# Performance work log

Hardware: AMD Instinct MI355X
Metric: run time of the kernel (lower is better)

Reference implementation:

```python
import jax, jax.numpy as jnp
import numpy as np

L, H, D, E, V, MAXS = 12, 12, 64, 768, 50257, 1024

def _ln(x, g, b, eps=1e-5):
    m = jnp.mean(x, axis=-1, keepdims=True)
    v = jnp.mean(jnp.square(x - m), axis=-1, keepdims=True)
    return (x - m) * jax.lax.rsqrt(v + eps) * g + b

def setup_inputs() -> dict:
    key = jax.random.key(0)
    ks = jax.random.split(key, 16)
    s = 0.02
    inp = {
        "input_ids": jax.random.randint(ks[0], (1, 1), 0, V),
        "past_key": jax.random.normal(ks[1], (L, 1, H, MAXS, D), jnp.float32),
        "past_value": jax.random.normal(ks[2], (L, 1, H, MAXS, D), jnp.float32),
        "past_seq_len": 1023,
        "attention_mask": jnp.ones((1, MAXS), jnp.float32),
        "wte": jax.random.normal(ks[3], (V, E), jnp.float32) * s,
        "wpe": jax.random.normal(ks[4], (MAXS, E), jnp.float32) * s,
        "ln1_g": jnp.ones((L, E), jnp.float32),
        "ln1_b": jnp.zeros((L, E), jnp.float32),
        "attn_w": jax.random.normal(ks[5], (L, E, 3 * E), jnp.float32) * s,
        "attn_b": jnp.zeros((L, 3 * E), jnp.float32),
        "proj_w": jax.random.normal(ks[6], (L, E, E), jnp.float32) * s,
        "proj_b": jnp.zeros((L, E), jnp.float32),
        "ln2_g": jnp.ones((L, E), jnp.float32),
        "ln2_b": jnp.zeros((L, E), jnp.float32),
        "fc_w": jax.random.normal(ks[7], (L, E, 4 * E), jnp.float32) * s,
        "fc_b": jnp.zeros((L, 4 * E), jnp.float32),
        "mlp_w": jax.random.normal(ks[8], (L, 4 * E, E), jnp.float32) * s,
        "mlp_b": jnp.zeros((L, E), jnp.float32),
        "lnf_g": jnp.ones((E,), jnp.float32),
        "lnf_b": jnp.zeros((E,), jnp.float32),
    }
    return inp

def reference(input_ids, past_key, past_value, past_seq_len, attention_mask,
              wte, wpe, ln1_g, ln1_b, attn_w, attn_b, proj_w, proj_b,
              ln2_g, ln2_b, fc_w, fc_b, mlp_w, mlp_b, lnf_g, lnf_b):
    S = int(past_seq_len)  # static cache length
    h = wte[input_ids] + wpe[S]                      # [1,1,E]
    bias = (1.0 - attention_mask[:, :S + 1]) * -1e9  # [1,S+1]
    scale = 1.0 / jnp.sqrt(jnp.float32(D))
    pk, pv = past_key, past_value
    for l in range(L):
        x = _ln(h, ln1_g[l], ln1_b[l])
        qkv = x @ attn_w[l] + attn_b[l]              # [1,1,3E]
        q, k, v = jnp.split(qkv, 3, axis=-1)
        q = q.reshape(1, 1, H, D).transpose(0, 2, 1, 3)  # [1,H,1,D]
        k = k.reshape(1, 1, H, D).transpose(0, 2, 1, 3)
        v = v.reshape(1, 1, H, D).transpose(0, 2, 1, 3)
        k_full = jnp.concatenate([pk[l, :, :, :S, :], k], axis=2)  # [1,H,S+1,D]
        v_full = jnp.concatenate([pv[l, :, :, :S, :], v], axis=2)
        scores = jnp.einsum('bhqd,bhkd->bhqk', q, k_full) * scale
        scores = scores + bias[:, None, None, :]
        attn = jax.nn.softmax(scores, axis=-1)
        o = jnp.einsum('bhqk,bhkd->bhqd', attn, v_full)
        o = o.transpose(0, 2, 1, 3).reshape(1, 1, H * D)
        h = h + o @ proj_w[l] + proj_b[l]
        x2 = _ln(h, ln2_g[l], ln2_b[l])
        h = h + jax.nn.gelu(x2 @ fc_w[l] + fc_b[l], approximate=True) @ mlp_w[l] + mlp_b[l]
        pk = pk.at[l, :, :, S, :].set(k[:, :, 0, :])
        pv = pv.at[l, :, :, S, :].set(v[:, :, 0, :])
    h = _ln(h, lnf_g, lnf_b)
    logits = h @ wte.T                               # [1,1,V] (tied lm_head)
    return (logits, pk, pv)
```

## Files before the change

### kernel.cpp

```cpp
#include <hip/hip_runtime.h>
#include <math.h>

#define EMB 768
#define NH 12
#define HD 64
#define NL 12
#define NV 50257
#define MAXS 1024
#define S_PAST 1023
#define E3 2304
#define E4 3072

#define WS_H    0
#define WS_QKV  768
#define WS_FC   3072
#define WS_PART 6144

__device__ __forceinline__ void blockReduce2(float& a, float& b, volatile float* ra, volatile float* rb) {
  int lane = threadIdx.x & 63, wid = threadIdx.x >> 6;
#pragma unroll
  for (int o = 32; o > 0; o >>= 1) { a += __shfl_down(a, o); b += __shfl_down(b, o); }
  if (lane == 0) { ra[wid] = a; rb[wid] = b; }
  __syncthreads();
  if (threadIdx.x == 0) {
    ra[0] = ra[0] + ra[1] + ra[2] + ra[3];
    rb[0] = rb[0] + rb[1] + rb[2] + rb[3];
  }
  __syncthreads();
  a = ra[0]; b = rb[0];
}

__global__ void embed_kernel(const int* __restrict__ ids, const float* __restrict__ wte,
                             const float* __restrict__ wpe, const float* __restrict__ attn_b,
                             float* __restrict__ hvec, float* __restrict__ qkv) {
  int idx = blockIdx.x * 256 + threadIdx.x;
  if (idx < E3) qkv[idx] = attn_b[idx];
  if (idx < EMB) {
    int id = ids[0];
    hvec[idx] = wte[(size_t)id * EMB + idx] + wpe[(size_t)S_PAST * EMB + idx];
  }
}

__global__ void ln_gemv4(const float* __restrict__ hvec, const float* __restrict__ g,
                         const float* __restrict__ bb, const float* __restrict__ W,
                         float* __restrict__ out, int N, int l) {
  __shared__ float lh[EMB];
  __shared__ float xs[64];
  __shared__ float ra[4], rb[4];
  __shared__ float4 red[4][64];
  int tid = threadIdx.x, lane = tid & 63, wid = tid >> 6;
  float s1 = 0.f, s2 = 0.f;
  for (int e = tid; e < EMB; e += 256) { float v = hvec[e]; lh[e] = v; s1 += v; s2 += v * v; }
  blockReduce2(s1, s2, ra, rb);
  float mean = s1 * (1.f / EMB);
  float var = s2 * (1.f / EMB) - mean * mean;
  float rstd = rsqrtf(var + 1e-5f);
  int e0 = blockIdx.y * 64;
  if (tid < 64) {
    int e = e0 + tid;
    xs[tid] = (lh[e] - mean) * rstd * g[l * EMB + e] + bb[l * EMB + e];
  }
  __syncthreads();
  int j4 = blockIdx.x * 64 + lane;
  int N4 = N >> 2;
  const float4* W4 = (const float4*)(W + (size_t)l * EMB * N) + (size_t)e0 * N4 + j4;
  const float4* p = W4 + (size_t)wid * N4;
  float4 w[16];
#pragma unroll
  for (int i = 0; i < 16; i++) w[i] = p[(size_t)(i * 4) * N4];
  float4 acc = {0.f, 0.f, 0.f, 0.f};
#pragma unroll
  for (int i = 0; i < 16; i++) {
    float x = xs[wid + i * 4];
    acc.x += x * w[i].x; acc.y += x * w[i].y; acc.z += x * w[i].z; acc.w += x * w[i].w;
  }
  red[wid][lane] = acc;
  __syncthreads();
  if (wid == 0) {
    float4 a0 = red[0][lane], a1 = red[1][lane], a2 = red[2][lane], a3 = red[3][lane];
    float rx = a0.x + a1.x + a2.x + a3.x;
    float ry = a0.y + a1.y + a2.y + a3.y;
    float rz = a0.z + a1.z + a2.z + a3.z;
    float rw = a0.w + a1.w + a2.w + a3.w;
    float* op = out + (size_t)j4 * 4;
    atomicAdd(op + 0, rx); atomicAdd(op + 1, ry);
    atomicAdd(op + 2, rz); atomicAdd(op + 3, rw);
  }
}

__global__ void attn_kv(const float* __restrict__ qkv, const float* __restrict__ pk,
                        const float* __restrict__ pv, const float* __restrict__ mask,
                        float* __restrict__ opk, float* __restrict__ opv,
                        float* __restrict__ part, int l) {
  int h = blockIdx.x >> 3, c = blockIdx.x & 7;
  int tid = threadIdx.x, lane = tid & 63, wid = tid >> 6;
  int sub = tid & 15, grp = tid >> 4;
  __shared__ float4 qs4[16];
  __shared__ float sc[128];
  __shared__ float4 redo[4][16];
  if (tid < 16) qs4[tid] = ((const float4*)(qkv + h * 64))[tid];
  __syncthreads();
  size_t base = ((size_t)(l * NH + h) * MAXS) * HD;
  const float4* K4 = (const float4*)(pk + base);
  const float4* V4 = (const float4*)(pv + base);
  float4* oK4 = (float4*)(opk + base);
  float4* oV4 = (float4*)(opv + base);
  int t0 = c * 128;
  float4 kreg[8];
#pragma unroll
  for (int i = 0; i < 8; i++) {
    int t = t0 + grp + i * 16;
    kreg[i] = (t == S_PAST) ? ((const float4*)(qkv + EMB + h * 64))[sub] : K4[(size_t)t * 16 + sub];
  }
#pragma unroll
  for (int i = 0; i < 8; i++) {
    int t = t0 + grp + i * 16;
    oK4[(size_t)t * 16 + sub] = kreg[i];
  }
  float4 q4 = qs4[sub];
#pragma unroll
  for (int i = 0; i < 8; i++) {
    int key = grp + i * 16;
    float p = q4.x * kreg[i].x + q4.y * kreg[i].y + q4.z * kreg[i].z + q4.w * kreg[i].w;
    p += __shfl_xor(p, 1); p += __shfl_xor(p, 2);
    p += __shfl_xor(p, 4); p += __shfl_xor(p, 8);
    if (sub == 0) sc[key] = p * 0.125f + (1.f - mask[t0 + key]) * (-1e9f);
  }
  __syncthreads();
  if (wid == 0) {
    float a = sc[lane], b2 = sc[lane + 64];
    float m = fmaxf(a, b2);
#pragma unroll
    for (int o = 32; o > 0; o >>= 1) m = fmaxf(m, __shfl_down(m, o));
    m = __shfl(m, 0);
    float ea = expf(a - m), eb = expf(b2 - m);
    sc[lane] = ea; sc[lane + 64] = eb;
    float s = ea + eb;
#pragma unroll
    for (int o = 32; o > 0; o >>= 1) s += __shfl_down(s, o);
    if (lane == 0) { part[(h * 8 + c) * 68 + 0] = m; part[(h * 8 + c) * 68 + 1] = s; }
  }
  __syncthreads();
  float4 vreg[8];
#pragma unroll
  for (int i = 0; i < 8; i++) {
    int t = t0 + grp + i * 16;
    vreg[i] = (t == S_PAST) ? ((const float4*)(qkv + 2 * EMB + h * 64))[sub] : V4[(size_t)t * 16 + sub];
  }
#pragma unroll
  for (int i = 0; i < 8; i++) {
    int t = t0 + grp + i * 16;
    oV4[(size_t)t * 16 + sub] = vreg[i];
  }
  float4 acc = {0.f, 0.f, 0.f, 0.f};
#pragma unroll
  for (int i = 0; i < 8; i++) {
    float w = sc[grp + i * 16];
    acc.x += w * vreg[i].x; acc.y += w * vreg[i].y; acc.z += w * vreg[i].z; acc.w += w * vreg[i].w;
  }
  acc.x += __shfl_xor(acc.x, 16); acc.y += __shfl_xor(acc.y, 16);
  acc.z += __shfl_xor(acc.z, 16); acc.w += __shfl_xor(acc.w, 16);
  acc.x += __shfl_xor(acc.x, 32); acc.y += __shfl_xor(acc.y, 32);
  acc.z += __shfl_xor(acc.z, 32); acc.w += __shfl_xor(acc.w, 32);
  if (lane < 16) redo[wid][lane] = acc;
  __syncthreads();
  if (tid < 16) {
    float4 a0 = redo[0][tid], a1 = redo[1][tid], a2 = redo[2][tid], a3 = redo[3][tid];
    float4 r;
    r.x = a0.x + a1.x + a2.x + a3.x;
    r.y = a0.y + a1.y + a2.y + a3.y;
    r.z = a0.z + a1.z + a2.z + a3.z;
    r.w = a0.w + a1.w + a2.w + a3.w;
    ((float4*)(part + (h * 8 + c) * 68 + 4))[tid] = r;
  }
}

__global__ void proj_attn(const float* __restrict__ part, const float* __restrict__ W,
                          const float* __restrict__ bias, const float* __restrict__ fc_b,
                          float* __restrict__ hout, float* __restrict__ wfc, int l) {
  int jb = blockIdx.x;
  int h = blockIdx.y;
  int tid = threadIdx.x, lane = tid & 63, wid = tid >> 6;
  __shared__ float xs[64];
  __shared__ float4 red[4][64];
  if (tid < 64) {
    float M = -1e30f;
    for (int cc = 0; cc < 8; cc++) M = fmaxf(M, part[(h * 8 + cc) * 68]);
    float T = 0.f, o = 0.f;
    for (int cc = 0; cc < 8; cc++) {
      float w = expf(part[(h * 8 + cc) * 68] - M);
      T += part[(h * 8 + cc) * 68 + 1] * w;
      o += part[(h * 8 + cc) * 68 + 4 + tid] * w;
    }
    xs[tid] = o / T;
  }
  int bid = h * 3 + jb;
  if (bid < 12) wfc[bid * 256 + tid] = fc_b[l * E4 + bid * 256 + tid];
  __syncthreads();
  int j4 = jb * 64 + lane;
  const int N4 = EMB >> 2;
  const float4* W4 = (const float4*)(W + (size_t)l * EMB * EMB) + (size_t)(h * 64) * N4 + j4;
  const float4* p = W4 + (size_t)wid * N4;
  float4 w[16];
#pragma unroll
  for (int i = 0; i < 16; i++) w[i] = p[(size_t)(i * 4) * N4];
  float4 acc = {0.f, 0.f, 0.f, 0.f};
#pragma unroll
  for (int i = 0; i < 16; i++) {
    float x = xs[wid + i * 4];
    acc.x += x * w[i].x; acc.y += x * w[i].y; acc.z += x * w[i].z; acc.w += x * w[i].w;
  }
  red[wid][lane] = acc;
  __syncthreads();
  if (wid == 0) {
    float4 a0 = red[0][lane], a1 = red[1][lane], a2 = red[2][lane], a3 = red[3][lane];
    float rx = a0.x + a1.x + a2.x + a3.x;
    float ry = a0.y + a1.y + a2.y + a3.y;
    float rz = a0.z + a1.z + a2.z + a3.z;
    float rw = a0.w + a1.w + a2.w + a3.w;
    if (h == 0) {
      const float* bp = bias + l * EMB + j4 * 4;
      rx += bp[0]; ry += bp[1]; rz += bp[2]; rw += bp[3];
    }
    float* op = hout + (size_t)j4 * 4;
    atomicAdd(op + 0, rx); atomicAdd(op + 1, ry);
    atomicAdd(op + 2, rz); atomicAdd(op + 3, rw);
  }
}

__global__ void mlp_gemv4(const float* __restrict__ fcv, const float* __restrict__ W,
                          const float* __restrict__ bias, const float* __restrict__ attn_b,
                          float* __restrict__ hout, float* __restrict__ qkv, int l) {
  __shared__ float xs[128];
  __shared__ float4 red[4][64];
  int tid = threadIdx.x, lane = tid & 63, wid = tid >> 6;
  int e0 = blockIdx.y * 128;
  if (tid < 128) {
    float x = fcv[e0 + tid];
    xs[tid] = 0.5f * x * (1.f + tanhf(0.7978845608028654f * (x + 0.044715f * x * x * x)));
  }
  int bid = blockIdx.y * 3 + blockIdx.x;
  if (l + 1 < NL && bid < 9) qkv[bid * 256 + tid] = attn_b[(l + 1) * E3 + bid * 256 + tid];
  __syncthreads();
  int j4 = blockIdx.x * 64 + lane;
  const int N4 = EMB >> 2;
  const float4* W4 = (const float4*)(W + (size_t)l * E4 * EMB) + (size_t)e0 * N4 + j4;
  float4 acc = {0.f, 0.f, 0.f, 0.f};
#pragma unroll
  for (int b = 0; b < 2; b++) {
    const float4* p = W4 + (size_t)(b * 64 + wid) * N4;
    float4 w[16];
#pragma unroll
    for (int i = 0; i < 16; i++) w[i] = p[(size_t)(i * 4) * N4];
#pragma unroll
    for (int i = 0; i < 16; i++) {
      float x = xs[b * 64 + wid + i * 4];
      acc.x += x * w[i].x; acc.y += x * w[i].y; acc.z += x * w[i].z; acc.w += x * w[i].w;
    }
  }
  red[wid][lane] = acc;
  __syncthreads();
  if (wid == 0) {
    float4 a0 = red[0][lane], a1 = red[1][lane], a2 = red[2][lane], a3 = red[3][lane];
    float rx = a0.x + a1.x + a2.x + a3.x;
    float ry = a0.y + a1.y + a2.y + a3.y;
    float rz = a0.z + a1.z + a2.z + a3.z;
    float rw = a0.w + a1.w + a2.w + a3.w;
    if (blockIdx.y == 0) {
      const float* bp = bias + l * EMB + j4 * 4;
      rx += bp[0]; ry += bp[1]; rz += bp[2]; rw += bp[3];
    }
    float* op = hout + (size_t)j4 * 4;
    atomicAdd(op + 0, rx); atomicAdd(op + 1, ry);
    atomicAdd(op + 2, rz); atomicAdd(op + 3, rw);
  }
}

__global__ void logits_lnf(const float* __restrict__ hvec, const float* __restrict__ g,
                           const float* __restrict__ b, const float* __restrict__ wte,
                           float* __restrict__ out) {
  __shared__ float4 xs4[192];
  __shared__ float ra[4], rb[4];
  int tid = threadIdx.x, lane = tid & 63, wid = tid >> 6;
  float s1 = 0.f, s2 = 0.f;
  float v0[3];
  int k = 0;
  for (int e = tid; e < EMB; e += 256, k++) { float v = hvec[e]; v0[k] = v; s1 += v; s2 += v * v; }
  blockReduce2(s1, s2, ra, rb);
  float mean = s1 * (1.f / EMB);
  float var = s2 * (1.f / EMB) - mean * mean;
  float rstd = rsqrtf(var + 1e-5f);
  k = 0;
  for (int e = tid; e < EMB; e += 256, k++)
    ((float*)xs4)[e] = (v0[k] - mean) * rstd * g[e] + b[e];
  __syncthreads();
  int v = blockIdx.x * 4 + wid;
  if (v >= NV) return;
  const float4* row = (const float4*)(wte + (size_t)v * EMB);
  float4 a0 = row[lane], a1 = row[lane + 64], a2 = row[lane + 128];
  float4 x0 = xs4[lane], x1 = xs4[lane + 64], x2 = xs4[lane + 128];
  float acc = a0.x * x0.x + a0.y * x0.y + a0.z * x0.z + a0.w * x0.w
            + a1.x * x1.x + a1.y * x1.y + a1.z * x1.z + a1.w * x1.w
            + a2.x * x2.x + a2.y * x2.y + a2.z * x2.z + a2.w * x2.w;
#pragma unroll
  for (int o = 32; o > 0; o >>= 1) acc += __shfl_down(acc, o);
  if (lane == 0) out[v] = acc;
}

extern "C" void kernel_launch(void* const* d_in, const int* in_sizes, int n_in,
                              void* d_out, int out_size, void* d_ws, size_t ws_size,
                              hipStream_t stream) {
  const int* input_ids = (const int*)d_in[0];
  const float* past_key = (const float*)d_in[1];
  const float* past_value = (const float*)d_in[2];
  const float* mask = (const float*)d_in[4];
  const float* wte = (const float*)d_in[5];
  const float* wpe = (const float*)d_in[6];
  const float* ln1_g = (const float*)d_in[7];
  const float* ln1_b = (const float*)d_in[8];
  const float* attn_w = (const float*)d_in[9];
  const float* attn_b = (const float*)d_in[10];
  const float* proj_w = (const float*)d_in[11];
  const float* proj_b = (const float*)d_in[12];
  const float* ln2_g = (const float*)d_in[13];
  const float* ln2_b = (const float*)d_in[14];
  const float* fc_w = (const float*)d_in[15];
  const float* fc_b = (const float*)d_in[16];
  const float* mlp_w = (const float*)d_in[17];
  const float* mlp_b = (const float*)d_in[18];
  const float* lnf_g = (const float*)d_in[19];
  const float* lnf_b = (const float*)d_in[20];

  float* out = (float*)d_out;
  float* out_logits = out;
  float* out_pk = out + NV;
  float* out_pv = out_pk + (size_t)NL * NH * MAXS * HD;

  float* ws = (float*)d_ws;
  float* wh = ws + WS_H;
  float* wqkv = ws + WS_QKV;
  float* wfc = ws + WS_FC;
  float* wpart = ws + WS_PART;

  embed_kernel<<<9, 256, 0, stream>>>(input_ids, wte, wpe, attn_b, wh, wqkv);

  for (int l = 0; l < NL; l++) {
    ln_gemv4<<<dim3(9, 12), 256, 0, stream>>>(wh, ln1_g, ln1_b, attn_w, wqkv, E3, l);
    attn_kv<<<96, 256, 0, stream>>>(wqkv, past_key, past_value, mask, out_pk, out_pv, wpart, l);
    proj_attn<<<dim3(3, 12), 256, 0, stream>>>(wpart, proj_w, proj_b, fc_b, wh, wfc, l);
    ln_gemv4<<<dim3(12, 12), 256, 0, stream>>>(wh, ln2_g, ln2_b, fc_w, wfc, E4, l);
    mlp_gemv4<<<dim3(3, 24), 256, 0, stream>>>(wfc, mlp_w, mlp_b, attn_b, wh, wqkv, l);
  }
  logits_lnf<<<12565, 256, 0, stream>>>(wh, lnf_g, lnf_b, wte, out_logits);
}
```

Before: 444.6 us.

## Bulk-copy KV cache upfront and split GEMV/attention across more blocks

Moves the full past KV cache copy into one bandwidth-bound kernel at the start, merged with the embedding setup. The per-layer attention kernel then only writes the new token's K/V row. All per-layer kernels (QKV, attention, projection, FC, MLP) now use smaller row chunks per block and roughly double or quadruple their grid sizes. This is meant to raise parallelism on the many CUs in the serial decode chain, at the cost of more atomic adds and partial results.

```diff
diff --git a/kernel.cpp b/kernel.cpp
--- a/kernel.cpp
+++ b/kernel.cpp
@@ -30,22 +30,39 @@
   a = ra[0]; b = rb[0];
 }
 
-__global__ void embed_kernel(const int* __restrict__ ids, const float* __restrict__ wte,
-                             const float* __restrict__ wpe, const float* __restrict__ attn_b,
-                             float* __restrict__ hvec, float* __restrict__ qkv) {
-  int idx = blockIdx.x * 256 + threadIdx.x;
-  if (idx < E3) qkv[idx] = attn_b[idx];
-  if (idx < EMB) {
-    int id = ids[0];
-    hvec[idx] = wte[(size_t)id * EMB + idx] + wpe[(size_t)S_PAST * EMB + idx];
-  }
-}
-
+__global__ void copy_embed(const float* __restrict__ pk, const float* __restrict__ pv,
+                           float* __restrict__ opk, float* __restrict__ opv,
+                           const int* __restrict__ ids, const float* __restrict__ wte,
+                           const float* __restrict__ wpe, const float* __restrict__ attn_b,
+                           float* __restrict__ hvec, float* __restrict__ qkv) {
+  int tid = threadIdx.x;
+  if (blockIdx.x >= 2048) {
+    int bi = blockIdx.x - 2048;
+    qkv[bi * 256 + tid] = attn_b[bi * 256 + tid];
+    if (bi < 3) {
+      int id = ids[0];
+      int e = bi * 256 + tid;
+      hvec[e] = wte[(size_t)id * EMB + e] + wpe[(size_t)S_PAST * EMB + e];
+    }
+    return;
+  }
+  const size_t n4 = (size_t)NL * NH * MAXS * HD / 4;
+  const float4* pk4 = (const float4*)pk;
+  const float4* pv4 = (const float4*)pv;
+  float4* opk4 = (float4*)opk;
+  float4* opv4 = (float4*)opv;
+  for (size_t i = (size_t)blockIdx.x * 256 + tid; i < n4; i += (size_t)2048 * 256) {
+    opk4[i] = pk4[i];
+    opv4[i] = pv4[i];
+  }
+}
+
+template<int R>
 __global__ void ln_gemv4(const float* __restrict__ hvec, const float* __restrict__ g,
                          const float* __restrict__ bb, const float* __restrict__ W,
                          float* __restrict__ out, int N, int l) {
   __shared__ float lh[EMB];
-  __shared__ float xs[64];
+  __shared__ float xs[R];
   __shared__ float ra[4], rb[4];
   __shared__ float4 red[4][64];
   int tid = threadIdx.x, lane = tid & 63, wid = tid >> 6;
@@ -55,22 +72,21 @@
   float mean = s1 * (1.f / EMB);
   float var = s2 * (1.f / EMB) - mean * mean;
   float rstd = rsqrtf(var + 1e-5f);
-  int e0 = blockIdx.y * 64;
-  if (tid < 64) {
+  int e0 = blockIdx.y * R;
+  if (tid < R) {
     int e = e0 + tid;
     xs[tid] = (lh[e] - mean) * rstd * g[l * EMB + e] + bb[l * EMB + e];
   }
   __syncthreads();
   int j4 = blockIdx.x * 64 + lane;
   int N4 = N >> 2;
-  const float4* W4 = (const float4*)(W + (size_t)l * EMB * N) + (size_t)e0 * N4 + j4;
-  const float4* p = W4 + (size_t)wid * N4;
-  float4 w[16];
-#pragma unroll
-  for (int i = 0; i < 16; i++) w[i] = p[(size_t)(i * 4) * N4];
+  const float4* p = (const float4*)(W + (size_t)l * EMB * N) + (size_t)e0 * N4 + j4 + (size_t)wid * N4;
+  float4 w[R / 4];
+#pragma unroll
+  for (int i = 0; i < R / 4; i++) w[i] = p[(size_t)(i * 4) * N4];
   float4 acc = {0.f, 0.f, 0.f, 0.f};
 #pragma unroll
-  for (int i = 0; i < 16; i++) {
+  for (int i = 0; i < R / 4; i++) {
     float x = xs[wid + i * 4];
     acc.x += x * w[i].x; acc.y += x * w[i].y; acc.z += x * w[i].z; acc.w += x * w[i].w;
   }
@@ -92,34 +108,29 @@
                         const float* __restrict__ pv, const float* __restrict__ mask,
                         float* __restrict__ opk, float* __restrict__ opv,
                         float* __restrict__ part, int l) {
-  int h = blockIdx.x >> 3, c = blockIdx.x & 7;
+  int h = blockIdx.x >> 4, c = blockIdx.x & 15;
   int tid = threadIdx.x, lane = tid & 63, wid = tid >> 6;
   int sub = tid & 15, grp = tid >> 4;
   __shared__ float4 qs4[16];
-  __shared__ float sc[128];
+  __shared__ float sc[64];
   __shared__ float4 redo[4][16];
   if (tid < 16) qs4[tid] = ((const float4*)(qkv + h * 64))[tid];
   __syncthreads();
   size_t base = ((size_t)(l * NH + h) * MAXS) * HD;
   const float4* K4 = (const float4*)(pk + base);
   const float4* V4 = (const float4*)(pv + base);
-  float4* oK4 = (float4*)(opk + base);
-  float4* oV4 = (float4*)(opv + base);
-  int t0 = c * 128;
-  float4 kreg[8];
-#pragma unroll
-  for (int i = 0; i < 8; i++) {
+  int t0 = c * 64;
+  float4 kreg[4];
+#pragma unroll
+  for (int i = 0; i < 4; i++) {
     int t = t0 + grp + i * 16;
     kreg[i] = (t == S_PAST) ? ((const float4*)(qkv + EMB + h * 64))[sub] : K4[(size_t)t * 16 + sub];
   }
-#pragma unroll
-  for (int i = 0; i < 8; i++) {
-    int t = t0 + grp + i * 16;
-    oK4[(size_t)t * 16 + sub] = kreg[i];
-  }
+  if (c == 15 && grp == 15)
+    ((float4*)(opk + base))[(size_t)S_PAST * 16 + sub] = kreg[3];
   float4 q4 = qs4[sub];
 #pragma unroll
-  for (int i = 0; i < 8; i++) {
+  for (int i = 0; i < 4; i++) {
     int key = grp + i * 16;
     float p = q4.x * kreg[i].x + q4.y * kreg[i].y + q4.z * kreg[i].z + q4.w * kreg[i].w;
     p += __shfl_xor(p, 1); p += __shfl_xor(p, 2);
@@ -128,33 +139,30 @@
   }
   __syncthreads();
   if (wid == 0) {
-    float a = sc[lane], b2 = sc[lane + 64];
-    float m = fmaxf(a, b2);
+    float a = sc[lane];
+    float m = a;
 #pragma unroll
     for (int o = 32; o > 0; o >>= 1) m = fmaxf(m, __shfl_down(m, o));
     m = __shfl(m, 0);
-    float ea = expf(a - m), eb = expf(b2 - m);
-    sc[lane] = ea; sc[lane + 64] = eb;
-    float s = ea + eb;
+    float ea = expf(a - m);
+    sc[lane] = ea;
+    float s = ea;
 #pragma unroll
     for (int o = 32; o > 0; o >>= 1) s += __shfl_down(s, o);
-    if (lane == 0) { part[(h * 8 + c) * 68 + 0] = m; part[(h * 8 + c) * 68 + 1] = s; }
-  }
-  __syncthreads();
-  float4 vreg[8];
-#pragma unroll
-  for (int i = 0; i < 8; i++) {
+    if (lane == 0) { part[(h * 16 + c) * 68 + 0] = m; part[(h * 16 + c) * 68 + 1] = s; }
+  }
+  __syncthreads();
+  float4 vreg[4];
+#pragma unroll
+  for (int i = 0; i < 4; i++) {
     int t = t0 + grp + i * 16;
     vreg[i] = (t == S_PAST) ? ((const float4*)(qkv + 2 * EMB + h * 64))[sub] : V4[(size_t)t * 16 + sub];
   }
-#pragma unroll
-  for (int i = 0; i < 8; i++) {
-    int t = t0 + grp + i * 16;
-    oV4[(size_t)t * 16 + sub] = vreg[i];
-  }
+  if (c == 15 && grp == 15)
+    ((float4*)(opv + base))[(size_t)S_PAST * 16 + sub] = vreg[3];
   float4 acc = {0.f, 0.f, 0.f, 0.f};
 #pragma unroll
-  for (int i = 0; i < 8; i++) {
+  for (int i = 0; i < 4; i++) {
     float w = sc[grp + i * 16];
     acc.x += w * vreg[i].x; acc.y += w * vreg[i].y; acc.z += w * vreg[i].z; acc.w += w * vreg[i].w;
   }
@@ -171,7 +179,7 @@
     r.y = a0.y + a1.y + a2.y + a3.y;
     r.z = a0.z + a1.z + a2.z + a3.z;
     r.w = a0.w + a1.w + a2.w + a3.w;
-    ((float4*)(part + (h * 8 + c) * 68 + 4))[tid] = r;
+    ((float4*)(part + (h * 16 + c) * 68 + 4))[tid] = r;
   }
 }
 
@@ -179,34 +187,38 @@
                           const float* __restrict__ bias, const float* __restrict__ fc_b,
                           float* __restrict__ hout, float* __restrict__ wfc, int l) {
   int jb = blockIdx.x;
-  int h = blockIdx.y;
-  int tid = threadIdx.x, lane = tid & 63, wid = tid >> 6;
-  __shared__ float xs[64];
+  int rt = blockIdx.y;
+  int h = rt >> 2, esub = rt & 3;
+  int tid = threadIdx.x, lane = tid & 63, wid = tid >> 6;
+  __shared__ float xs[16];
   __shared__ float4 red[4][64];
-  if (tid < 64) {
+  if (tid < 16) {
     float M = -1e30f;
-    for (int cc = 0; cc < 8; cc++) M = fmaxf(M, part[(h * 8 + cc) * 68]);
+#pragma unroll
+    for (int cc = 0; cc < 16; cc++) M = fmaxf(M, part[(h * 16 + cc) * 68]);
     float T = 0.f, o = 0.f;
-    for (int cc = 0; cc < 8; cc++) {
-      float w = expf(part[(h * 8 + cc) * 68] - M);
-      T += part[(h * 8 + cc) * 68 + 1] * w;
-      o += part[(h * 8 + cc) * 68 + 4 + tid] * w;
+    int d = esub * 16 + tid;
+#pragma unroll
+    for (int cc = 0; cc < 16; cc++) {
+      float w = expf(part[(h * 16 + cc) * 68] - M);
+      T += part[(h * 16 + cc) * 68 + 1] * w;
+      o += part[(h * 16 + cc) * 68 + 4 + d] * w;
     }
     xs[tid] = o / T;
   }
-  int bid = h * 3 + jb;
+  int bid = rt * 3 + jb;
   if (bid < 12) wfc[bid * 256 + tid] = fc_b[l * E4 + bid * 256 + tid];
   __syncthreads();
   int j4 = jb * 64 + lane;
   const int N4 = EMB >> 2;
-  const float4* W4 = (const float4*)(W + (size_t)l * EMB * EMB) + (size_t)(h * 64) * N4 + j4;
-  const float4* p = W4 + (size_t)wid * N4;
-  float4 w[16];
-#pragma unroll
-  for (int i = 0; i < 16; i++) w[i] = p[(size_t)(i * 4) * N4];
+  int r0 = h * 64 + esub * 16;
+  const float4* p = (const float4*)(W + (size_t)l * EMB * EMB) + (size_t)(r0 + wid) * N4 + j4;
+  float4 w[4];
+#pragma unroll
+  for (int i = 0; i < 4; i++) w[i] = p[(size_t)(i * 4) * N4];
   float4 acc = {0.f, 0.f, 0.f, 0.f};
 #pragma unroll
-  for (int i = 0; i < 16; i++) {
+  for (int i = 0; i < 4; i++) {
     float x = xs[wid + i * 4];
     acc.x += x * w[i].x; acc.y += x * w[i].y; acc.z += x * w[i].z; acc.w += x * w[i].w;
   }
@@ -218,11 +230,11 @@
     float ry = a0.y + a1.y + a2.y + a3.y;
     float rz = a0.z + a1.z + a2.z + a3.z;
     float rw = a0.w + a1.w + a2.w + a3.w;
-    if (h == 0) {
-      const float* bp = bias + l * EMB + j4 * 4;
+    if (rt == 0) {
+      const float* bp = bias + l * EMB + jb * 256 + lane * 4;
       rx += bp[0]; ry += bp[1]; rz += bp[2]; rw += bp[3];
     }
-    float* op = hout + (size_t)j4 * 4;
+    float* op = hout + (size_t)jb * 256 + (size_t)lane * 4;
     atomicAdd(op + 0, rx); atomicAdd(op + 1, ry);
     atomicAdd(op + 2, rz); atomicAdd(op + 3, rw);
   }
@@ -231,11 +243,11 @@
 __global__ void mlp_gemv4(const float* __restrict__ fcv, const float* __restrict__ W,
                           const float* __restrict__ bias, const float* __restrict__ attn_b,
                           float* __restrict__ hout, float* __restrict__ qkv, int l) {
-  __shared__ float xs[128];
+  __shared__ float xs[64];
   __shared__ float4 red[4][64];
   int tid = threadIdx.x, lane = tid & 63, wid = tid >> 6;
-  int e0 = blockIdx.y * 128;
-  if (tid < 128) {
+  int e0 = blockIdx.y * 64;
+  if (tid < 64) {
     float x = fcv[e0 + tid];
     xs[tid] = 0.5f * x * (1.f + tanhf(0.7978845608028654f * (x + 0.044715f * x * x * x)));
   }
@@ -244,19 +256,15 @@
   __syncthreads();
   int j4 = blockIdx.x * 64 + lane;
   const int N4 = EMB >> 2;
-  const float4* W4 = (const float4*)(W + (size_t)l * E4 * EMB) + (size_t)e0 * N4 + j4;
+  const float4* p = (const float4*)(W + (size_t)l * E4 * EMB) + (size_t)(e0 + wid) * N4 + j4;
+  float4 w[16];
+#pragma unroll
+  for (int i = 0; i < 16; i++) w[i] = p[(size_t)(i * 4) * N4];
   float4 acc = {0.f, 0.f, 0.f, 0.f};
 #pragma unroll
-  for (int b = 0; b < 2; b++) {
-    const float4* p = W4 + (size_t)(b * 64 + wid) * N4;
-    float4 w[16];
-#pragma unroll
-    for (int i = 0; i < 16; i++) w[i] = p[(size_t)(i * 4) * N4];
-#pragma unroll
-    for (int i = 0; i < 16; i++) {
-      float x = xs[b * 64 + wid + i * 4];
-      acc.x += x * w[i].x; acc.y += x * w[i].y; acc.z += x * w[i].z; acc.w += x * w[i].w;
-    }
+  for (int i = 0; i < 16; i++) {
+    float x = xs[wid + i * 4];
+    acc.x += x * w[i].x; acc.y += x * w[i].y; acc.z += x * w[i].z; acc.w += x * w[i].w;
   }
   red[wid][lane] = acc;
   __syncthreads();
@@ -342,14 +350,15 @@
   float* wfc = ws + WS_FC;
   float* wpart = ws + WS_PART;
 
-  embed_kernel<<<9, 256, 0, stream>>>(input_ids, wte, wpe, attn_b, wh, wqkv);
+  copy_embed<<<2057, 256, 0, stream>>>(past_key, past_value, out_pk, out_pv,
+                                       input_ids, wte, wpe, attn_b, wh, wqkv);
 
   for (int l = 0; l < NL; l++) {
-    ln_gemv4<<<dim3(9, 12), 256, 0, stream>>>(wh, ln1_g, ln1_b, attn_w, wqkv, E3, l);
-    attn_kv<<<96, 256, 0, stream>>>(wqkv, past_key, past_value, mask, out_pk, out_pv, wpart, l);
-    proj_attn<<<dim3(3, 12), 256, 0, stream>>>(wpart, proj_w, proj_b, fc_b, wh, wfc, l);
-    ln_gemv4<<<dim3(12, 12), 256, 0, stream>>>(wh, ln2_g, ln2_b, fc_w, wfc, E4, l);
-    mlp_gemv4<<<dim3(3, 24), 256, 0, stream>>>(wfc, mlp_w, mlp_b, attn_b, wh, wqkv, l);
+    ln_gemv4<32><<<dim3(9, 24), 256, 0, stream>>>(wh, ln1_g, ln1_b, attn_w, wqkv, E3, l);
+    attn_kv<<<192, 256, 0, stream>>>(wqkv, past_key, past_value, mask, out_pk, out_pv, wpart, l);
+    proj_attn<<<dim3(3, 48), 256, 0, stream>>>(wpart, proj_w, proj_b, fc_b, wh, wfc, l);
+    ln_gemv4<32><<<dim3(12, 24), 256, 0, stream>>>(wh, ln2_g, ln2_b, fc_w, wfc, E4, l);
+    mlp_gemv4<<<dim3(3, 48), 256, 0, stream>>>(wfc, mlp_w, mlp_b, attn_b, wh, wqkv, l);
   }
   logits_lnf<<<12565, 256, 0, stream>>>(wh, lnf_g, lnf_b, wte, out_logits);
 }
```

Measured after the change: 498.5 us. 12.1% more time.
